# Optimization experiments

Hardware: AMD Instinct MI355X
Metric: run time of the kernel (lower is better)

The kernel has to match this reference:

```python
import jax, jax.numpy as jnp
import numpy as np

DEPTH, DIM, DIN, DM, NST, RNK, CSTEM, NCLS = 4, 64, 128, 256, 16, 8, 32, 16
EPS = 1e-5


def silu(x):
    return x * jax.nn.sigmoid(x)


def layernorm(x, g, b):
    m = x.mean(-1, keepdims=True)
    v = x.var(-1, keepdims=True)
    return (x - m) / jnp.sqrt(v + EPS) * g + b


def bn3d(x, g, b, m, v):  # eval-mode BatchNorm3d, x [B,C,T,H,W]
    s = g / jnp.sqrt(v + EPS)
    return x * s[None, :, None, None, None] + (b - m * s)[None, :, None, None, None]


def dwconv3d_same(x, w, b):  # x [B,C,T,H,W], w [C,1,3,3,3]
    y = jax.lax.conv_general_dilated(x, w, (1, 1, 1), 'SAME',
                                     feature_group_count=x.shape[1],
                                     dimension_numbers=('NCDHW', 'OIDHW', 'NCDHW'))
    return y + b[None, :, None, None, None]


def mamba(u, in_w, conv_w, conv_b, xproj_w, dtproj_w, dtproj_b, Alog, Dp, out_w):
    # u: [b, L, DIN]; mamba_ssm Mamba(d_model=DIN, d_state=16, expand=2, d_conv=4)
    b, L, _ = u.shape
    xz = u @ in_w.T                                  # [b,L,2*DM]
    x, z = jnp.split(xz, 2, axis=-1)                 # [b,L,DM] each
    # causal depthwise conv1d, kernel 4, left-pad 3
    xc = jnp.moveaxis(x, 1, 2)                       # [b,DM,L]
    xc = jnp.pad(xc, ((0, 0), (0, 0), (3, 0)))
    xc = jax.lax.conv_general_dilated(xc, conv_w, (1,), 'VALID',
                                      feature_group_count=conv_w.shape[0],
                                      dimension_numbers=('NCH', 'OIH', 'NCH'))
    xc = xc + conv_b[None, :, None]
    x = silu(jnp.moveaxis(xc, 2, 1))                 # [b,L,DM]
    dbc = x @ xproj_w.T                              # [b,L,RNK+2*NST]
    dt, Bc, Cc = jnp.split(dbc, [RNK, RNK + NST], axis=-1)
    dt = jax.nn.softplus(dt @ dtproj_w.T + dtproj_b)  # [b,L,DM]
    A = -jnp.exp(Alog)                               # [DM,NST]

    def step(h, inp):
        dt_l, u_l, B_l, C_l = inp                    # [b,DM],[b,DM],[b,NST],[b,NST]
        dA = jnp.exp(dt_l[..., None] * A)            # [b,DM,NST]
        h = dA * h + (dt_l * u_l)[..., None] * B_l[:, None, :]
        y = jnp.einsum('bdn,bn->bd', h, C_l)
        return h, y

    xs = (jnp.moveaxis(dt, 1, 0), jnp.moveaxis(x, 1, 0),
          jnp.moveaxis(Bc, 1, 0), jnp.moveaxis(Cc, 1, 0))
    h0 = jnp.zeros((b, DM, NST), x.dtype)
    _, ys = jax.lax.scan(step, h0, xs)               # ys [L,b,DM]
    y = jnp.moveaxis(ys, 0, 1) + x * Dp              # D skip
    y = y * silu(z)
    return y @ out_w.T                               # [b,L,DIN]


def setup_inputs() -> dict:
    key = jax.random.key(0)
    ks = iter(jax.random.split(key, 64))

    def rn(shape, s=0.02):
        return jax.random.normal(next(ks), shape, jnp.float32) * s

    D = DEPTH
    inp = {
        'x': jax.random.normal(next(ks), (32, 1, 32, 13, 13), jnp.float32),
        # R(2+1)D stem
        'sconv_w': rn((CSTEM, 1, 1, 3, 3), 0.1),
        'bn1_g': jnp.ones((CSTEM,)), 'bn1_b': jnp.zeros((CSTEM,)),
        'bn1_m': rn((CSTEM,), 0.1),
        'bn1_v': jax.random.uniform(next(ks), (CSTEM,), jnp.float32, 0.5, 1.5),
        'tconv_w': rn((CSTEM, 1, 3, 1, 1), 0.2),
        'bn2_g': jnp.ones((CSTEM,)), 'bn2_b': jnp.zeros((CSTEM,)),
        'bn2_m': rn((CSTEM,), 0.1),
        'bn2_v': jax.random.uniform(next(ks), (CSTEM,), jnp.float32, 0.5, 1.5),
        'last_w': rn((2 * CSTEM, CSTEM, 1, 1, 1), 0.1),
        # per-block params, stacked over depth
        'ln1_g': jnp.ones((D, DIM)), 'ln1_b': jnp.zeros((D, DIM)),
        'in_proj_w': rn((D, 2 * DIN, DIM)),
        'conv3d_w': rn((D, DIN, 1, 3, 3, 3), 0.1), 'conv3d_b': rn((D, DIN), 0.1),
        'm_in_w': rn((D, 2 * DM, DIN)),
        'm_conv_w': rn((D, DM, 1, 4), 0.2), 'm_conv_b': rn((D, DM), 0.1),
        'm_xproj_w': rn((D, RNK + 2 * NST, DM)),
        'm_dtproj_w': rn((D, DM, RNK), 0.1), 'm_dtproj_b': rn((D, DM), 0.1),
        'm_Alog': jnp.log(jax.random.uniform(next(ks), (D, DM, NST), jnp.float32, 1.0, 16.0)),
        'm_D': jnp.ones((D, DM)),
        'm_out_w': rn((D, DIN, DM)),
        'out_proj_w': rn((D, DIM, DIN)),
        'ln2_g': jnp.ones((D, DIM)), 'ln2_b': jnp.zeros((D, DIM)),
        'fc1_w': rn((D, 4 * DIM, DIM)), 'fc1_b': rn((D, 4 * DIM), 0.1),
        'fc2_w': rn((D, DIM, 4 * DIM)), 'fc2_b': rn((D, DIM), 0.1),
        'head_w': rn((NCLS, DIM)), 'head_b': jnp.zeros((NCLS,)),
    }
    return inp


def reference(x, sconv_w, bn1_g, bn1_b, bn1_m, bn1_v, tconv_w, bn2_g, bn2_b, bn2_m,
              bn2_v, last_w, ln1_g, ln1_b, in_proj_w, conv3d_w, conv3d_b, m_in_w,
              m_conv_w, m_conv_b, m_xproj_w, m_dtproj_w, m_dtproj_b, m_Alog, m_D,
              m_out_w, out_proj_w, ln2_g, ln2_b, fc1_w, fc1_b, fc2_w, fc2_b,
              head_w, head_b):
    dn = ('NCDHW', 'OIDHW', 'NCDHW')
    # R(2+1)D stem: spatial conv -> BN -> ReLU -> temporal dwconv -> BN -> ReLU -> 1x1x1
    h = jax.lax.conv_general_dilated(x, sconv_w, (1, 1, 1), 'VALID', dimension_numbers=dn)
    h = jax.nn.relu(bn3d(h, bn1_g, bn1_b, bn1_m, bn1_v))
    h = jax.lax.conv_general_dilated(h, tconv_w, (1, 1, 1), 'VALID',
                                     feature_group_count=CSTEM, dimension_numbers=dn)
    h = jax.nn.relu(bn3d(h, bn2_g, bn2_b, bn2_m, bn2_v))
    h = jax.lax.conv_general_dilated(h, last_w, (1, 1, 1), 'VALID', dimension_numbers=dn)
    xb = jnp.transpose(h, (0, 2, 3, 4, 1))  # [B, T', H', W', DIM]

    for i in range(DEPTH):
        # --- SSM branch ---
        hx = layernorm(xb, ln1_g[i], ln1_b[i])
        xz = hx @ in_proj_w[i].T                       # [B,T,H,W,2*DIN]
        xs_, z = jnp.split(xz, 2, axis=-1)
        z = silu(z)
        xc = jnp.moveaxis(xs_, 4, 1)                   # [B,DIN,T,H,W]
        xc = silu(dwconv3d_same(xc, conv3d_w[i], conv3d_b[i]))
        b, c, t, hh, ww = xc.shape
        seq = jnp.moveaxis(xc.reshape(b, c, t * hh * ww), 1, 2)  # [B,L,DIN]
        seq2 = jnp.concatenate([seq, seq[:, ::-1]], axis=0)      # [2B,L,DIN]
        y2 = mamba(seq2, m_in_w[i], m_conv_w[i], m_conv_b[i], m_xproj_w[i],
                   m_dtproj_w[i], m_dtproj_b[i], m_Alog[i], m_D[i], m_out_w[i])
        y = y2[:b] + y2[b:, ::-1]
        y = y.reshape(b, t, hh, ww, c) * z
        xb = xb + y @ out_proj_w[i].T
        # --- MLP branch ---
        h2 = layernorm(xb, ln2_g[i], ln2_b[i])
        h2 = jax.nn.gelu(h2 @ fc1_w[i].T + fc1_b[i], approximate=False)
        xb = xb + h2 @ fc2_w[i].T + fc2_b[i]

    feature = xb.mean(axis=(1, 2, 3))                  # [B, DIM]
    logits = feature @ head_w.T + head_b               # [B, NCLS]
    return (logits, feature)
```

## Files before the change

kernel.cpp:

```cpp
#include <hip/hip_runtime.h>
#include <hip/hip_bf16.h>
#include <hip/hip_fp16.h>

#define LL    3630
#define EPSV  1e-5f
#define NCH   33
#define CLEN  110

typedef short bf16x8 __attribute__((ext_vector_type(8)));
typedef float f32x4  __attribute__((ext_vector_type(4)));
typedef float f32x2  __attribute__((ext_vector_type(2)));
typedef float f32x16 __attribute__((ext_vector_type(16)));

__device__ __forceinline__ float bf2f(__hip_bfloat16 x){ return __bfloat162float(x); }
__device__ __forceinline__ __hip_bfloat16 f2bf(float x){ return __float2bfloat16(x); }
__device__ __forceinline__ float siluf(float x){ return x / (1.f + __expf(-x)); }
__device__ __forceinline__ float s2f(short s){ __hip_bfloat16 t = __builtin_bit_cast(__hip_bfloat16, s); return __bfloat162float(t); }
__device__ __forceinline__ short f2s(float x){ __hip_bfloat16 t = __float2bfloat16(x); return __builtin_bit_cast(short, t); }

__global__ __launch_bounds__(256) void convert_weights(
    const float* __restrict__ s0, const float* __restrict__ s1,
    const float* __restrict__ s2, const float* __restrict__ s3,
    const float* __restrict__ s4, const float* __restrict__ s5,
    const float* __restrict__ s6,
    __hip_bfloat16* __restrict__ dst)
{
  int gid = blockIdx.x*256 + threadIdx.x;
  float v;
  if      (gid <  65536) v = s0[gid];
  else if (gid < 327680) v = s1[gid-65536];
  else if (gid < 458752) v = s2[gid-327680];
  else if (gid < 491520) v = s3[gid-458752];
  else if (gid < 557056) v = s4[gid-491520];
  else if (gid < 622592) v = s5[gid-557056];
  else if (gid < 671744){
    int rel = gid - 622592;
    int layer = rel / 12288;
    int rr  = (rel % 12288) / 256;
    int ccol= rel & 255;
    v = (rr < 40) ? s6[layer*10240 + rr*256 + ccol] : 0.f;
  }
  else return;
  dst[gid] = f2bf(v);
}

__global__ __launch_bounds__(256) void stem1_kernel(
    const float* __restrict__ x, const float* __restrict__ w,
    const float* __restrict__ g, const float* __restrict__ bb,
    const float* __restrict__ mm, const float* __restrict__ vv,
    float* __restrict__ out, int nb, int b0)
{
  int idx = blockIdx.x*256 + threadIdx.x;
  if (idx >= nb*123904) return;
  int j = idx % 11;
  int i = (idx/11) % 11;
  int t = (idx/121) % 32;
  int c = (idx/(121*32)) % 32;
  int b = idx/(121*32*32);
  const float* xp = x + ((b0+b)*32 + t)*169;
  const float* wp = w + c*9;
  float acc = 0.f;
  #pragma unroll
  for (int di=0; di<3; ++di)
    #pragma unroll
    for (int dj=0; dj<3; ++dj)
      acc += xp[(i+di)*13 + (j+dj)] * wp[di*3+dj];
  float s = g[c]*rsqrtf(vv[c]+EPSV);
  acc = acc*s + (bb[c]-mm[c]*s);
  out[idx] = fmaxf(acc, 0.f);
}

__global__ __launch_bounds__(256) void stem2_kernel(
    const float* __restrict__ h1, const float* __restrict__ w,
    const float* __restrict__ g, const float* __restrict__ bb,
    const float* __restrict__ mm, const float* __restrict__ vv,
    float* __restrict__ out, int nb)
{
  int idx = blockIdx.x*256 + threadIdx.x;
  if (idx >= nb*116160) return;
  int ij = idx % 121;
  int t  = (idx/121) % 30;
  int c  = (idx/(121*30)) % 32;
  int b  = idx/(121*30*32);
  const float* hp = h1 + ((b*32+c)*32)*121 + ij;
  const float* wp = w + c*3;
  float acc = 0.f;
  #pragma unroll
  for (int k=0;k<3;++k) acc += hp[(t+k)*121] * wp[k];
  float s = g[c]*rsqrtf(vv[c]+EPSV);
  acc = acc*s + (bb[c]-mm[c]*s);
  out[idx] = fmaxf(acc, 0.f);
}

__global__ __launch_bounds__(256) void stem3_kernel(
    const float* __restrict__ h2, const float* __restrict__ w,
    __hip_bfloat16* __restrict__ xb, int tokens)
{
  int gid = blockIdx.x*256 + threadIdx.x;
  int cc = gid & 63;
  int tok = gid >> 6;
  if (tok >= tokens) return;
  int ij = tok % 121;
  int t  = (tok/121) % 30;
  int b  = tok/LL;
  const float* hp = h2 + ((long)b*32)*30*121 + t*121 + ij;
  const float* wp = w + cc*32;
  float acc = 0.f;
  #pragma unroll
  for (int ci=0; ci<32; ++ci) acc += hp[ci*3630] * wp[ci];
  xb[(long)tok*64+cc] = f2bf(acc);
}

__global__ __launch_bounds__(256) void ln_kernel(
    const __hip_bfloat16* __restrict__ xb, const float* __restrict__ g,
    const float* __restrict__ b2, __hip_bfloat16* __restrict__ out, int tokens)
{
  int wid = threadIdx.x >> 6, lane = threadIdx.x & 63;
  long tok = (long)blockIdx.x*4 + wid;
  if (tok >= tokens) return;
  float v = bf2f(xb[tok*64 + lane]);
  float s = v, q = v*v;
  #pragma unroll
  for (int m=1; m<64; m<<=1){ s += __shfl_xor(s,m); q += __shfl_xor(q,m); }
  float mean = s*(1.f/64.f);
  float var  = q*(1.f/64.f) - mean*mean;
  float o = (v-mean)*rsqrtf(var+EPSV)*g[lane] + b2[lane];
  out[tok*64+lane] = f2bf(o);
}

template<int EPI>
__global__ __launch_bounds__(256) void gemm_bf16(
    const __hip_bfloat16* __restrict__ A, const __hip_bfloat16* __restrict__ W,
    int K, int N, int NH, int tokens,
    __hip_bfloat16* __restrict__ out1, __hip_bfloat16* __restrict__ out2,
    const float* __restrict__ bias, const __hip_bfloat16* __restrict__ gate,
    __hip_bfloat16* __restrict__ resid,
    const float* __restrict__ lng, const float* __restrict__ lnb)
{
  int w   = threadIdx.x >> 6;
  int lane= threadIdx.x & 63;
  int r16 = lane & 15;
  int kg  = lane >> 4;
  long m0 = (long)blockIdx.x*128 + w*32;
  int  n0 = blockIdx.y*64;
  long ra0 = m0 + r16;      if (ra0 > tokens-1) ra0 = tokens-1;
  long ra1 = m0 + 16 + r16; if (ra1 > tokens-1) ra1 = tokens-1;
  f32x4 acc[2][4] = { { {0,0,0,0},{0,0,0,0},{0,0,0,0},{0,0,0,0} },
                      { {0,0,0,0},{0,0,0,0},{0,0,0,0},{0,0,0,0} } };
  for (int k0 = 0; k0 < K; k0 += 32){
    bf16x8 a0 = *reinterpret_cast<const bf16x8*>(A + ra0*K + k0 + kg*8);
    bf16x8 a1 = *reinterpret_cast<const bf16x8*>(A + ra1*K + k0 + kg*8);
    #pragma unroll
    for (int f=0; f<4; ++f){
      bf16x8 b = *reinterpret_cast<const bf16x8*>(W + (long)(n0 + f*16 + r16)*K + k0 + kg*8);
      acc[0][f] = __builtin_amdgcn_mfma_f32_16x16x32_bf16(a0, b, acc[0][f], 0, 0, 0);
      acc[1][f] = __builtin_amdgcn_mfma_f32_16x16x32_bf16(a1, b, acc[1][f], 0, 0, 0);
    }
  }
  if (EPI == 5){
    float gv[4], bv[4], biasv[4];
    #pragma unroll
    for (int f=0; f<4; ++f){
      gv[f] = lng[f*16+r16]; bv[f] = lnb[f*16+r16];
      biasv[f] = bias ? bias[f*16+r16] : 0.f;
    }
    #pragma unroll
    for (int g2=0; g2<2; ++g2){
      #pragma unroll
      for (int r=0; r<4; ++r){
        long row = m0 + g2*16 + kg*4 + r;
        bool ok = row < tokens;
        long rowc = ok ? row : (tokens-1);
        float v[4]; float s = 0.f, q = 0.f;
        #pragma unroll
        for (int f=0; f<4; ++f){
          float t = acc[g2][f][r] + biasv[f] + bf2f(resid[rowc*64 + f*16+r16]);
          v[f] = t; s += t; q += t*t;
        }
        #pragma unroll
        for (int m=1; m<16; m<<=1){ s += __shfl_xor(s,m); q += __shfl_xor(q,m); }
        float mean = s*(1.f/64.f);
        float var  = q*(1.f/64.f) - mean*mean;
        float rstd = rsqrtf(var+EPSV);
        if (ok){
          #pragma unroll
          for (int f=0; f<4; ++f){
            resid[row*64 + f*16+r16] = f2bf(v[f]);
            out1 [row*64 + f*16+r16] = f2bf((v[f]-mean)*rstd*gv[f] + bv[f]);
          }
        }
      }
    }
    return;
  }
  #pragma unroll
  for (int g2=0; g2<2; ++g2){
    #pragma unroll
    for (int f=0; f<4; ++f){
      int col = n0 + f*16 + r16;
      #pragma unroll
      for (int r=0; r<4; ++r){
        long row = m0 + g2*16 + kg*4 + r;
        if (row >= tokens) continue;
        float v = acc[g2][f][r];
        if (EPI == 0){
          if (col < NH) out1[row*NH + col] = f2bf(v);
          else          out2[row*NH + col - NH] = f2bf(siluf(v));
        } else if (EPI == 2){
          v += bias[col];
          v = 0.5f*v*(1.f + erff(v*0.70710678118f));
          out1[row*N + col] = f2bf(v);
        } else if (EPI == 3){
          if (bias) v += bias[col];
          resid[row*N + col] = f2bf(v + bf2f(resid[row*N + col]));
        } else {
          out1[row*N + col] = f2bf(v * bf2f(gate[row*N + col]));
        }
      }
    }
  }
}

__global__ __launch_bounds__(256) void dwconv3d_kernel(
    const __hip_bfloat16* __restrict__ xs, const float* __restrict__ w,
    const float* __restrict__ bias, __hip_bfloat16* __restrict__ seq, int tokens)
{
  long gid = (long)blockIdx.x*256 + threadIdx.x;
  int c = gid & 127;
  long tok = gid >> 7;
  if (tok >= tokens) return;
  int j  = tok % 11;
  int i2 = (tok/11) % 11;
  int t  = (tok/121) % 30;
  long b = tok/LL;
  const float* wc = w + c*27;
  float acc = bias[c];
  #pragma unroll
  for (int dt=0; dt<3; ++dt){
    int tt = t+dt-1; if (tt<0 || tt>=30) continue;
    #pragma unroll
    for (int di=0; di<3; ++di){
      int ii = i2+di-1; if (ii<0 || ii>=11) continue;
      #pragma unroll
      for (int dj=0; dj<3; ++dj){
        int jj = j+dj-1; if (jj<0 || jj>=11) continue;
        long t2 = (b*30+tt)*121 + ii*11 + jj;
        acc += wc[dt*9+di*3+dj] * bf2f(xs[t2*128 + c]);
      }
    }
  }
  seq[tok*128 + c] = f2bf(siluf(acc));
}

__global__ __launch_bounds__(256) void mamba_pre_kernel(
    const __hip_bfloat16* __restrict__ xm,
    const float* __restrict__ cw, const float* __restrict__ cbv,
    const __hip_bfloat16* __restrict__ xpw_bf,
    __hip_bfloat16* __restrict__ ub,
    float* __restrict__ pre,
    int nb)
{
  __shared__ __hip_bfloat16 xcs[64][264];
  int s  = blockIdx.x / 57;
  int ch = blockIdx.x % 57;
  int p0 = ch*64;
  int b  = s % nb;
  bool fwd = s < nb;
  int d = threadIdx.x;
  const long basex = (long)b*LL*256 + d;
  const long sLL = (long)s*LL;
  float w0=cw[d*4], w1=cw[d*4+1], w2=cw[d*4+2], w3=cw[d*4+3], cb=cbv[d];
  float p1=0.f, p2=0.f, p3=0.f;
  if (p0-1 >= 0) p1 = bf2f(xm[basex + (long)(fwd ? p0-1 : LL-p0  )*256]);
  if (p0-2 >= 0) p2 = bf2f(xm[basex + (long)(fwd ? p0-2 : LL+1-p0)*256]);
  if (p0-3 >= 0) p3 = bf2f(xm[basex + (long)(fwd ? p0-3 : LL+2-p0)*256]);
  for (int t=0; t<64; ++t){
    int p = p0 + t;
    float xl = 0.f;
    if (p < LL) xl = bf2f(xm[basex + (long)(fwd ? p : LL-1-p)*256]);
    float xc = w3*xl + w2*p1 + w1*p2 + w0*p3 + cb;
    p3=p2; p2=p1; p1=xl;
    __hip_bfloat16 uv = f2bf(siluf(xc));
    xcs[t][d] = uv;
    if (p < LL) ub[(sLL + p)*256 + d] = uv;
  }
  __syncthreads();
  int w = threadIdx.x >> 6, lane = threadIdx.x & 63;
  int r16 = lane & 15, kg = lane >> 4;
  int t0 = w*16;
  f32x4 acc[3] = { {0,0,0,0},{0,0,0,0},{0,0,0,0} };
  for (int k0=0; k0<256; k0+=32){
    bf16x8 a = *reinterpret_cast<const bf16x8*>(&xcs[t0+r16][k0+kg*8]);
    #pragma unroll
    for (int f=0; f<3; ++f){
      bf16x8 bb = *reinterpret_cast<const bf16x8*>(xpw_bf + (f*16+r16)*256 + k0 + kg*8);
      acc[f] = __builtin_amdgcn_mfma_f32_16x16x32_bf16(a, bb, acc[f], 0, 0, 0);
    }
  }
  #pragma unroll
  for (int f=0; f<3; ++f){
    int col = f*16 + r16;
    #pragma unroll
    for (int r=0; r<4; ++r){
      int tl = t0 + kg*4 + r;
      int p = p0 + tl;
      if (p >= LL) continue;
      if (col < 40) pre[(sLL + p)*40 + col] = acc[f][r];
    }
  }
}

__global__ __launch_bounds__(256) void scan_p1(
    const __hip_bfloat16* __restrict__ ub,
    const float* __restrict__ pre,
    const float* __restrict__ dtw, const float* __restrict__ dtbv,
    const float* __restrict__ Alog,
    float* __restrict__ hfin, float* __restrict__ sdt)
{
  int d = threadIdx.x;
  int sc = blockIdx.x;
  int ch = sc % NCH, s = sc / NCH;
  f32x2 a2[8], h[8];
  #pragma unroll
  for (int k=0;k<8;++k){
    a2[k] = (f32x2){ -__expf(Alog[d*16+2*k])*1.44269504f,
                     -__expf(Alog[d*16+2*k+1])*1.44269504f };
    h[k] = (f32x2){0.f, 0.f};
  }
  float dw[8];
  #pragma unroll
  for (int r=0;r<8;++r) dw[r] = dtw[d*8+r];
  float dtb_d = dtbv[d];
  float sacc = 0.f;
  long tok0 = (long)s*LL + ch*CLEN;
  long ui = tok0*256 + d;
  long pi = tok0*40;
  for (int l=0; l<CLEN; ++l){
    float u = bf2f(ub[ui]);
    float4 r0 = *reinterpret_cast<const float4*>(pre+pi);
    float4 r1 = *reinterpret_cast<const float4*>(pre+pi+4);
    float xacc = dtb_d;
    xacc = fmaf(r0.x,dw[0],fmaf(r0.y,dw[1],fmaf(r0.z,dw[2],fmaf(r0.w,dw[3],xacc))));
    xacc = fmaf(r1.x,dw[4],fmaf(r1.y,dw[5],fmaf(r1.z,dw[6],fmaf(r1.w,dw[7],xacc))));
    float dt = (xacc > 20.f) ? xacc : __logf(1.f + __expf(xacc));
    sacc += dt;
    f32x16 B = *reinterpret_cast<const f32x16*>(pre+pi+8);
    f32x2 dt2  = (f32x2){dt, dt};
    float dtu = dt*u;
    f32x2 dtu2 = (f32x2){dtu, dtu};
    #pragma unroll
    for (int k=0;k<8;++k){
      f32x2 t = dt2*a2[k];
      f32x2 e = (f32x2){ exp2f(t.x), exp2f(t.y) };
      f32x2 bk = (f32x2){ B[2*k], B[2*k+1] };
      h[k] = __builtin_elementwise_fma(e, h[k], dtu2*bk);
    }
    ui += 256; pi += 40;
  }
  long hbase = ((long)sc*256 + d)*16;
  #pragma unroll
  for (int k=0;k<8;++k){ hfin[hbase+2*k] = h[k].x; hfin[hbase+2*k+1] = h[k].y; }
  sdt[(long)sc*256 + d] = sacc;
}

__global__ __launch_bounds__(256) void scan_comb(
    const float* __restrict__ Alog,
    float* __restrict__ hfin, const float* __restrict__ sdt)
{
  int s = blockIdx.x >> 4, dg = blockIdx.x & 15;
  int d = dg*16 + (threadIdx.x >> 4), n = threadIdx.x & 15;
  float a2 = -__expf(Alog[d*16+n]) * 1.44269504f;
  float h = 0.f;
  for (int ch=0; ch<NCH; ++ch){
    long sc = (long)s*NCH + ch;
    long idx = (sc*256 + d)*16 + n;
    float hf = hfin[idx];
    float sd = sdt[sc*256 + d];
    hfin[idx] = h;
    h = exp2f(a2*sd)*h + hf;
  }
}

__global__ __launch_bounds__(256) void scan_p2(
    __hip_bfloat16* __restrict__ ub,
    const float* __restrict__ pre,
    const float* __restrict__ dtw, const float* __restrict__ dtbv,
    const float* __restrict__ Alog, const float* __restrict__ Dv,
    const float* __restrict__ hinit)
{
  int d = threadIdx.x;
  int sc = blockIdx.x;
  int ch = sc % NCH, s = sc / NCH;
  f32x2 a2[8], h[8];
  long hbase = ((long)sc*256 + d)*16;
  #pragma unroll
  for (int k=0;k<8;++k){
    a2[k] = (f32x2){ -__expf(Alog[d*16+2*k])*1.44269504f,
                     -__expf(Alog[d*16+2*k+1])*1.44269504f };
    h[k] = (f32x2){ hinit[hbase+2*k], hinit[hbase+2*k+1] };
  }
  float dw[8];
  #pragma unroll
  for (int r=0;r<8;++r) dw[r] = dtw[d*8+r];
  float dtb_d = dtbv[d];
  float dpv = Dv[d];
  int l0 = ch*CLEN;
  long tok0 = (long)s*LL + l0;
  long ui = tok0*256 + d;
  long pi = tok0*40;
  for (int l=0; l<CLEN; ++l){
    float u = bf2f(ub[ui]);
    float4 r0 = *reinterpret_cast<const float4*>(pre+pi);
    float4 r1 = *reinterpret_cast<const float4*>(pre+pi+4);
    float xacc = dtb_d;
    xacc = fmaf(r0.x,dw[0],fmaf(r0.y,dw[1],fmaf(r0.z,dw[2],fmaf(r0.w,dw[3],xacc))));
    xacc = fmaf(r1.x,dw[4],fmaf(r1.y,dw[5],fmaf(r1.z,dw[6],fmaf(r1.w,dw[7],xacc))));
    float dt = (xacc > 20.f) ? xacc : __logf(1.f + __expf(xacc));
    f32x16 B = *reinterpret_cast<const f32x16*>(pre+pi+8);
    f32x16 C = *reinterpret_cast<const f32x16*>(pre+pi+24);
    f32x2 dt2  = (f32x2){dt, dt};
    float dtu = dt*u;
    f32x2 dtu2 = (f32x2){dtu, dtu};
    f32x2 y2 = (f32x2){0.f, 0.f};
    #pragma unroll
    for (int k=0;k<8;++k){
      f32x2 t = dt2*a2[k];
      f32x2 e = (f32x2){ exp2f(t.x), exp2f(t.y) };
      f32x2 bk = (f32x2){ B[2*k], B[2*k+1] };
      f32x2 ck = (f32x2){ C[2*k], C[2*k+1] };
      h[k] = __builtin_elementwise_fma(e, h[k], dtu2*bk);
      y2 = __builtin_elementwise_fma(h[k], ck, y2);
    }
    float y = y2.x + y2.y;
    ub[ui] = f2bf(y + u*dpv);
    ui += 256; pi += 40;
  }
}

__global__ __launch_bounds__(256) void combine_kernel(
    const __hip_bfloat16* __restrict__ yb, const __hip_bfloat16* __restrict__ zm,
    __hip_bfloat16* __restrict__ ycomb, int tokens, int nb)
{
  long gid = (long)blockIdx.x*256 + threadIdx.x;
  long tok = gid >> 5;
  if (tok >= tokens) return;
  int c8 = (gid & 31) * 8;
  long l = tok % LL, b = tok / LL;
  bf16x8 vf = *reinterpret_cast<const bf16x8*>(yb + ( b*LL + l)*256 + c8);
  bf16x8 vb = *reinterpret_cast<const bf16x8*>(yb + ((nb+b)*LL + (LL-1-l))*256 + c8);
  bf16x8 zz = *reinterpret_cast<const bf16x8*>(zm + tok*256 + c8);
  bf16x8 out;
  #pragma unroll
  for (int k=0;k<8;++k){
    float r = (s2f(vf[k]) + s2f(vb[k])) * s2f(zz[k]);
    out[k] = f2s(r);
  }
  *reinterpret_cast<bf16x8*>(ycomb + tok*256 + c8) = out;
}

__global__ __launch_bounds__(256) void head1_kernel(
    const __hip_bfloat16* __restrict__ xb, float* __restrict__ hp)
{
  __shared__ float partial[4][64];
  int b = blockIdx.x / 30, ch = blockIdx.x % 30;
  int d = threadIdx.x & 63, part = threadIdx.x >> 6;
  float acc = 0.f;
  int lend = (ch+1)*121;
  for (int l = ch*121 + part; l < lend; l += 4)
    acc += bf2f(xb[((long)b*LL + l)*64 + d]);
  partial[part][d] = acc;
  __syncthreads();
  if (part == 0)
    hp[(b*30 + ch)*64 + d] = partial[0][d]+partial[1][d]+partial[2][d]+partial[3][d];
}

__global__ __launch_bounds__(64) void head2_kernel(
    const float* __restrict__ hp, const float* __restrict__ hw,
    const float* __restrict__ hb, float* __restrict__ out, int b0)
{
  __shared__ float feat[64];
  int b = blockIdx.x;
  int d = threadIdx.x;
  float acc = 0.f;
  #pragma unroll
  for (int ch=0; ch<30; ++ch) acc += hp[(b*30+ch)*64 + d];
  float f = acc * (1.f/3630.f);
  feat[d] = f;
  out[512 + (b0+b)*64 + d] = f;
  __syncthreads();
  if (d < 16){
    float a2 = hb[d];
    #pragma unroll
    for (int k=0; k<64; ++k) a2 += feat[k]*hw[d*64+k];
    out[(b0+b)*16 + d] = a2;
  }
}

extern "C" void kernel_launch(void* const* d_in, const int* in_sizes, int n_in,
                              void* d_out, int out_size, void* d_ws, size_t ws_size,
                              hipStream_t stream)
{
  const float* x        = (const float*)d_in[0];
  const float* sconv_w  = (const float*)d_in[1];
  const float* bn1_g    = (const float*)d_in[2];
  const float* bn1_b    = (const float*)d_in[3];
  const float* bn1_m    = (const float*)d_in[4];
  const float* bn1_v    = (const float*)d_in[5];
  const float* tconv_w  = (const float*)d_in[6];
  const float* bn2_g    = (const float*)d_in[7];
  const float* bn2_b    = (const float*)d_in[8];
  const float* bn2_m    = (const float*)d_in[9];
  const float* bn2_v    = (const float*)d_in[10];
  const float* last_w   = (const float*)d_in[11];
  const float* ln1_g    = (const float*)d_in[12];
  const float* ln1_b    = (const float*)d_in[13];
  const float* in_proj_w= (const float*)d_in[14];
  const float* conv3d_w = (const float*)d_in[15];
  const float* conv3d_b = (const float*)d_in[16];
  const float* m_in_w   = (const float*)d_in[17];
  const float* m_conv_w = (const float*)d_in[18];
  const float* m_conv_b = (const float*)d_in[19];
  const float* m_xproj_w= (const float*)d_in[20];
  const float* m_dtproj_w=(const float*)d_in[21];
  const float* m_dtproj_b=(const float*)d_in[22];
  const float* m_Alog   = (const float*)d_in[23];
  const float* m_D      = (const float*)d_in[24];
  const float* m_out_w  = (const float*)d_in[25];
  const float* out_proj_w=(const float*)d_in[26];
  const float* ln2_g    = (const float*)d_in[27];
  const float* ln2_b    = (const float*)d_in[28];
  const float* fc1_w    = (const float*)d_in[29];
  const float* fc1_b    = (const float*)d_in[30];
  const float* fc2_w    = (const float*)d_in[31];
  const float* fc2_b    = (const float*)d_in[32];
  const float* head_w   = (const float*)d_in[33];
  const float* head_b   = (const float*)d_in[34];

  const size_t WB = 1345536;
  int nb = 1;
  for (int cand = 32; cand >= 1; cand >>= 1){
    size_t TPc = (((size_t)cand*LL + 63)/64)*64;
    size_t S2c = (size_t)2*cand*LL;
    size_t need = WB + TPc*2048 + S2c*672;
    if (need <= ws_size){ nb = cand; break; }
  }
  const size_t TP  = (((size_t)nb*LL + 63)/64)*64;
  const int S2  = 2*nb;
  const size_t S2T = (size_t)S2*LL;
  const int tokens = nb*LL;

  char* ws = (char*)d_ws;
  __hip_bfloat16* wbf   = (__hip_bfloat16*)(ws);
  size_t o = WB;
  __hip_bfloat16* xb    = (__hip_bfloat16*)(ws + o); o += TP*128;
  __hip_bfloat16* hx    = (__hip_bfloat16*)(ws + o); o += TP*128;
  float*          hp    = (float*)hx;
  __hip_bfloat16* xs    = (__hip_bfloat16*)(ws + o); o += TP*256;
  __hip_bfloat16* seq   = (__hip_bfloat16*)(ws + o); o += TP*256;
  __hip_bfloat16* ycomb = xs;
  float*          hfin  = (float*)xs;
  __hip_bfloat16* zblk  = (__hip_bfloat16*)(ws + o); o += TP*256;
  __hip_bfloat16* xm    = (__hip_bfloat16*)(ws + o);
  __hip_bfloat16* yo    = xm;                        o += TP*512;
  __hip_bfloat16* zm    = (__hip_bfloat16*)(ws + o);
  __hip_bfloat16* h2m   = zm;                        o += TP*512;
  float*          pre   = (float*)(ws + o);          o += S2T*160;
  __hip_bfloat16* ybuf  = (__hip_bfloat16*)(ws + o);
  float*          h1s   = (float*)(ws + o);
  float*          h2s   = (float*)(ws + o + (size_t)nb*495616);
  float*          sdtb  = hfin + (size_t)S2*NCH*4096;

  convert_weights<<<2624, 256, 0, stream>>>(in_proj_w, m_in_w, m_out_w, out_proj_w,
                                            fc1_w, fc2_w, m_xproj_w, wbf);

  const int gM2 = (int)((TP + 127)/128);

  for (int b0 = 0; b0 < 32; b0 += nb){
    stem1_kernel<<<nb*484, 256, 0, stream>>>(x, sconv_w, bn1_g, bn1_b, bn1_m, bn1_v, h1s, nb, b0);
    stem2_kernel<<<(nb*116160+255)/256, 256, 0, stream>>>(h1s, tconv_w, bn2_g, bn2_b, bn2_m, bn2_v, h2s, nb);
    stem3_kernel<<<(tokens*64+255)/256, 256, 0, stream>>>(h2s, last_w, xb, tokens);
    ln_kernel<<<(tokens+3)/4, 256, 0, stream>>>(xb, ln1_g, ln1_b, hx, tokens);

    for (int i = 0; i < 4; ++i){
      gemm_bf16<0><<<dim3(gM2,4), 256, 0, stream>>>(hx, wbf + i*16384, 64, 256, 128, tokens,
                                                    xs, zblk, nullptr, nullptr, nullptr, nullptr, nullptr);
      dwconv3d_kernel<<<(tokens*128+255)/256, 256, 0, stream>>>(xs, conv3d_w + i*3456, conv3d_b + i*128, seq, tokens);
      gemm_bf16<0><<<dim3(gM2,8), 256, 0, stream>>>(seq, wbf + 65536 + i*65536, 128, 512, 256, tokens,
                                                    xm, zm, nullptr, nullptr, nullptr, nullptr, nullptr);
      mamba_pre_kernel<<<S2*57, 256, 0, stream>>>(xm, m_conv_w + i*1024, m_conv_b + i*256,
                                                  wbf + 622592 + i*12288, ybuf, pre, nb);
      scan_p1<<<S2*NCH, 256, 0, stream>>>(ybuf, pre, m_dtproj_w + i*2048, m_dtproj_b + i*256,
                                          m_Alog + i*4096, hfin, sdtb);
      scan_comb<<<S2*16, 256, 0, stream>>>(m_Alog + i*4096, hfin, sdtb);
      scan_p2<<<S2*NCH, 256, 0, stream>>>(ybuf, pre, m_dtproj_w + i*2048, m_dtproj_b + i*256,
                                          m_Alog + i*4096, m_D + i*256, hfin);
      combine_kernel<<<(tokens*32+255)/256, 256, 0, stream>>>(ybuf, zm, ycomb, tokens, nb);
      gemm_bf16<4><<<dim3(gM2,2), 256, 0, stream>>>(ycomb, wbf + 327680 + i*32768, 256, 128, 0, tokens,
                                                    yo, nullptr, nullptr, zblk, nullptr, nullptr, nullptr);
      gemm_bf16<5><<<dim3(gM2,1), 256, 0, stream>>>(yo, wbf + 458752 + i*8192, 128, 64, 0, tokens,
                                                    hx, nullptr, nullptr, nullptr, xb,
                                                    ln2_g + i*64, ln2_b + i*64);
      gemm_bf16<2><<<dim3(gM2,4), 256, 0, stream>>>(hx, wbf + 491520 + i*16384, 64, 256, 0, tokens,
                                                    h2m, nullptr, fc1_b + i*256, nullptr, nullptr, nullptr, nullptr);
      int inext = (i < 3) ? i+1 : 3;
      gemm_bf16<5><<<dim3(gM2,1), 256, 0, stream>>>(h2m, wbf + 557056 + i*16384, 256, 64, 0, tokens,
                                                    hx, nullptr, fc2_b + i*64, nullptr, xb,
                                                    ln1_g + inext*64, ln1_b + inext*64);
    }
    head1_kernel<<<nb*30, 256, 0, stream>>>(xb, hp);
    head2_kernel<<<nb, 64, 0, stream>>>(hp, head_w, head_b, (float*)d_out, b0);
  }
}
```

Before: 6.706 ms.

## Fuse mamba pre-projection with chunked scan phase one using shared-memory inputs

Merges the conv1d+x_proj kernel with the first pass of the chunked selective scan. The scan now reads u and the dt/B projections from shared memory instead of global memory. Chunk length changes from 110 to 64 to match the pre-kernel tiling, giving 57 chunks per sequence. This removes a launch and a global re-read of ub/pre. In exchange it lengthens the sequential scan_comb pass and enlarges the hfin buffer, which is moved to alias a different workspace region.

After: 6.192 ms. 7.7% less time.

```diff
diff --git a/kernel.cpp b/kernel.cpp
--- a/kernel.cpp
+++ b/kernel.cpp
@@ -4,8 +4,8 @@
 
 #define LL    3630
 #define EPSV  1e-5f
-#define NCH   33
-#define CLEN  110
+#define NCH   57
+#define CLEN  64
 
 typedef short bf16x8 __attribute__((ext_vector_type(8)));
 typedef float f32x4  __attribute__((ext_vector_type(4)));
@@ -252,115 +252,118 @@
   seq[tok*128 + c] = f2bf(siluf(acc));
 }
 
-__global__ __launch_bounds__(256) void mamba_pre_kernel(
+__global__ __launch_bounds__(256) void mamba_pre_scan(
     const __hip_bfloat16* __restrict__ xm,
     const float* __restrict__ cw, const float* __restrict__ cbv,
     const __hip_bfloat16* __restrict__ xpw_bf,
+    const float* __restrict__ dtw, const float* __restrict__ dtbv,
+    const float* __restrict__ Alog,
     __hip_bfloat16* __restrict__ ub,
     float* __restrict__ pre,
+    float* __restrict__ hfin, float* __restrict__ sdt,
     int nb)
 {
   __shared__ __hip_bfloat16 xcs[64][264];
-  int s  = blockIdx.x / 57;
-  int ch = blockIdx.x % 57;
-  int p0 = ch*64;
+  __shared__ float pres[64][44];
+  int s  = blockIdx.x / NCH;
+  int ch = blockIdx.x % NCH;
+  int p0 = ch*CLEN;
   int b  = s % nb;
   bool fwd = s < nb;
   int d = threadIdx.x;
   const long basex = (long)b*LL*256 + d;
   const long sLL = (long)s*LL;
-  float w0=cw[d*4], w1=cw[d*4+1], w2=cw[d*4+2], w3=cw[d*4+3], cb=cbv[d];
-  float p1=0.f, p2=0.f, p3=0.f;
-  if (p0-1 >= 0) p1 = bf2f(xm[basex + (long)(fwd ? p0-1 : LL-p0  )*256]);
-  if (p0-2 >= 0) p2 = bf2f(xm[basex + (long)(fwd ? p0-2 : LL+1-p0)*256]);
-  if (p0-3 >= 0) p3 = bf2f(xm[basex + (long)(fwd ? p0-3 : LL+2-p0)*256]);
-  for (int t=0; t<64; ++t){
-    int p = p0 + t;
-    float xl = 0.f;
-    if (p < LL) xl = bf2f(xm[basex + (long)(fwd ? p : LL-1-p)*256]);
-    float xc = w3*xl + w2*p1 + w1*p2 + w0*p3 + cb;
-    p3=p2; p2=p1; p1=xl;
-    __hip_bfloat16 uv = f2bf(siluf(xc));
-    xcs[t][d] = uv;
-    if (p < LL) ub[(sLL + p)*256 + d] = uv;
+  {
+    float w0=cw[d*4], w1=cw[d*4+1], w2=cw[d*4+2], w3=cw[d*4+3], cb=cbv[d];
+    float p1=0.f, p2=0.f, p3=0.f;
+    if (p0-1 >= 0) p1 = bf2f(xm[basex + (long)(fwd ? p0-1 : LL-p0  )*256]);
+    if (p0-2 >= 0) p2 = bf2f(xm[basex + (long)(fwd ? p0-2 : LL+1-p0)*256]);
+    if (p0-3 >= 0) p3 = bf2f(xm[basex + (long)(fwd ? p0-3 : LL+2-p0)*256]);
+    for (int t=0; t<64; ++t){
+      int p = p0 + t;
+      float xl = 0.f;
+      if (p < LL) xl = bf2f(xm[basex + (long)(fwd ? p : LL-1-p)*256]);
+      float xc = w3*xl + w2*p1 + w1*p2 + w0*p3 + cb;
+      p3=p2; p2=p1; p1=xl;
+      __hip_bfloat16 uv = f2bf(siluf(xc));
+      xcs[t][d] = uv;
+      if (p < LL) ub[(sLL + p)*256 + d] = uv;
+    }
   }
   __syncthreads();
-  int w = threadIdx.x >> 6, lane = threadIdx.x & 63;
-  int r16 = lane & 15, kg = lane >> 4;
-  int t0 = w*16;
-  f32x4 acc[3] = { {0,0,0,0},{0,0,0,0},{0,0,0,0} };
-  for (int k0=0; k0<256; k0+=32){
-    bf16x8 a = *reinterpret_cast<const bf16x8*>(&xcs[t0+r16][k0+kg*8]);
+  {
+    int w = threadIdx.x >> 6, lane = threadIdx.x & 63;
+    int r16 = lane & 15, kg = lane >> 4;
+    int t0 = w*16;
+    f32x4 acc[3] = { {0,0,0,0},{0,0,0,0},{0,0,0,0} };
+    for (int k0=0; k0<256; k0+=32){
+      bf16x8 a = *reinterpret_cast<const bf16x8*>(&xcs[t0+r16][k0+kg*8]);
+      #pragma unroll
+      for (int f=0; f<3; ++f){
+        bf16x8 bb = *reinterpret_cast<const bf16x8*>(xpw_bf + (f*16+r16)*256 + k0 + kg*8);
+        acc[f] = __builtin_amdgcn_mfma_f32_16x16x32_bf16(a, bb, acc[f], 0, 0, 0);
+      }
+    }
     #pragma unroll
     for (int f=0; f<3; ++f){
-      bf16x8 bb = *reinterpret_cast<const bf16x8*>(xpw_bf + (f*16+r16)*256 + k0 + kg*8);
-      acc[f] = __builtin_amdgcn_mfma_f32_16x16x32_bf16(a, bb, acc[f], 0, 0, 0);
-    }
-  }
-  #pragma unroll
-  for (int f=0; f<3; ++f){
-    int col = f*16 + r16;
-    #pragma unroll
-    for (int r=0; r<4; ++r){
-      int tl = t0 + kg*4 + r;
-      int p = p0 + tl;
-      if (p >= LL) continue;
-      if (col < 40) pre[(sLL + p)*40 + col] = acc[f][r];
-    }
-  }
-}
-
-__global__ __launch_bounds__(256) void scan_p1(
-    const __hip_bfloat16* __restrict__ ub,
-    const float* __restrict__ pre,
-    const float* __restrict__ dtw, const float* __restrict__ dtbv,
-    const float* __restrict__ Alog,
-    float* __restrict__ hfin, float* __restrict__ sdt)
-{
-  int d = threadIdx.x;
-  int sc = blockIdx.x;
-  int ch = sc % NCH, s = sc / NCH;
-  f32x2 a2[8], h[8];
-  #pragma unroll
-  for (int k=0;k<8;++k){
-    a2[k] = (f32x2){ -__expf(Alog[d*16+2*k])*1.44269504f,
-                     -__expf(Alog[d*16+2*k+1])*1.44269504f };
-    h[k] = (f32x2){0.f, 0.f};
-  }
-  float dw[8];
-  #pragma unroll
-  for (int r=0;r<8;++r) dw[r] = dtw[d*8+r];
-  float dtb_d = dtbv[d];
-  float sacc = 0.f;
-  long tok0 = (long)s*LL + ch*CLEN;
-  long ui = tok0*256 + d;
-  long pi = tok0*40;
-  for (int l=0; l<CLEN; ++l){
-    float u = bf2f(ub[ui]);
-    float4 r0 = *reinterpret_cast<const float4*>(pre+pi);
-    float4 r1 = *reinterpret_cast<const float4*>(pre+pi+4);
-    float xacc = dtb_d;
-    xacc = fmaf(r0.x,dw[0],fmaf(r0.y,dw[1],fmaf(r0.z,dw[2],fmaf(r0.w,dw[3],xacc))));
-    xacc = fmaf(r1.x,dw[4],fmaf(r1.y,dw[5],fmaf(r1.z,dw[6],fmaf(r1.w,dw[7],xacc))));
-    float dt = (xacc > 20.f) ? xacc : __logf(1.f + __expf(xacc));
-    sacc += dt;
-    f32x16 B = *reinterpret_cast<const f32x16*>(pre+pi+8);
-    f32x2 dt2  = (f32x2){dt, dt};
-    float dtu = dt*u;
-    f32x2 dtu2 = (f32x2){dtu, dtu};
+      int col = f*16 + r16;
+      #pragma unroll
+      for (int r=0; r<4; ++r){
+        int tl = t0 + kg*4 + r;
+        int p = p0 + tl;
+        if (col < 40){
+          pres[tl][col] = acc[f][r];
+          if (p < LL) pre[(sLL + p)*40 + col] = acc[f][r];
+        }
+      }
+    }
+  }
+  __syncthreads();
+  {
+    int lim = LL - p0; if (lim > CLEN) lim = CLEN;
+    f32x2 a2[8], h[8];
     #pragma unroll
     for (int k=0;k<8;++k){
-      f32x2 t = dt2*a2[k];
-      f32x2 e = (f32x2){ exp2f(t.x), exp2f(t.y) };
-      f32x2 bk = (f32x2){ B[2*k], B[2*k+1] };
-      h[k] = __builtin_elementwise_fma(e, h[k], dtu2*bk);
-    }
-    ui += 256; pi += 40;
-  }
-  long hbase = ((long)sc*256 + d)*16;
-  #pragma unroll
-  for (int k=0;k<8;++k){ hfin[hbase+2*k] = h[k].x; hfin[hbase+2*k+1] = h[k].y; }
-  sdt[(long)sc*256 + d] = sacc;
+      a2[k] = (f32x2){ -__expf(Alog[d*16+2*k])*1.44269504f,
+                       -__expf(Alog[d*16+2*k+1])*1.44269504f };
+      h[k] = (f32x2){0.f, 0.f};
+    }
+    float dw[8];
+    #pragma unroll
+    for (int r=0;r<8;++r) dw[r] = dtw[d*8+r];
+    float dtb_d = dtbv[d];
+    float sacc = 0.f;
+    for (int t=0; t<lim; ++t){
+      float u = bf2f(xcs[t][d]);
+      float4 r0 = *reinterpret_cast<const float4*>(&pres[t][0]);
+      float4 r1 = *reinterpret_cast<const float4*>(&pres[t][4]);
+      float xacc = dtb_d;
+      xacc = fmaf(r0.x,dw[0],fmaf(r0.y,dw[1],fmaf(r0.z,dw[2],fmaf(r0.w,dw[3],xacc))));
+      xacc = fmaf(r1.x,dw[4],fmaf(r1.y,dw[5],fmaf(r1.z,dw[6],fmaf(r1.w,dw[7],xacc))));
+      float dt = (xacc > 20.f) ? xacc : __logf(1.f + __expf(xacc));
+      sacc += dt;
+      float4 B0 = *reinterpret_cast<const float4*>(&pres[t][8]);
+      float4 B1 = *reinterpret_cast<const float4*>(&pres[t][12]);
+      float4 B2 = *reinterpret_cast<const float4*>(&pres[t][16]);
+      float4 B3 = *reinterpret_cast<const float4*>(&pres[t][20]);
+      float Bv[16] = {B0.x,B0.y,B0.z,B0.w,B1.x,B1.y,B1.z,B1.w,
+                      B2.x,B2.y,B2.z,B2.w,B3.x,B3.y,B3.z,B3.w};
+      f32x2 dt2  = (f32x2){dt, dt};
+      float dtu = dt*u;
+      f32x2 dtu2 = (f32x2){dtu, dtu};
+      #pragma unroll
+      for (int k=0;k<8;++k){
+        f32x2 tt = dt2*a2[k];
+        f32x2 e = (f32x2){ exp2f(tt.x), exp2f(tt.y) };
+        f32x2 bk = (f32x2){ Bv[2*k], Bv[2*k+1] };
+        h[k] = __builtin_elementwise_fma(e, h[k], dtu2*bk);
+      }
+    }
+    long hbase = ((long)blockIdx.x*256 + d)*16;
+    #pragma unroll
+    for (int k=0;k<8;++k){ hfin[hbase+2*k] = h[k].x; hfin[hbase+2*k+1] = h[k].y; }
+    sdt[(long)blockIdx.x*256 + d] = sacc;
+  }
 }
 
 __global__ __launch_bounds__(256) void scan_comb(
@@ -391,6 +394,8 @@
   int d = threadIdx.x;
   int sc = blockIdx.x;
   int ch = sc % NCH, s = sc / NCH;
+  int l0 = ch*CLEN;
+  int lim = LL - l0; if (lim > CLEN) lim = CLEN;
   f32x2 a2[8], h[8];
   long hbase = ((long)sc*256 + d)*16;
   #pragma unroll
@@ -404,11 +409,10 @@
   for (int r=0;r<8;++r) dw[r] = dtw[d*8+r];
   float dtb_d = dtbv[d];
   float dpv = Dv[d];
-  int l0 = ch*CLEN;
   long tok0 = (long)s*LL + l0;
   long ui = tok0*256 + d;
   long pi = tok0*40;
-  for (int l=0; l<CLEN; ++l){
+  for (int l=0; l<lim; ++l){
     float u = bf2f(ub[ui]);
     float4 r0 = *reinterpret_cast<const float4*>(pre+pi);
     float4 r1 = *reinterpret_cast<const float4*>(pre+pi+4);
@@ -555,10 +559,10 @@
   __hip_bfloat16* xb    = (__hip_bfloat16*)(ws + o); o += TP*128;
   __hip_bfloat16* hx    = (__hip_bfloat16*)(ws + o); o += TP*128;
   float*          hp    = (float*)hx;
+  float*          hfin  = (float*)hx;
   __hip_bfloat16* xs    = (__hip_bfloat16*)(ws + o); o += TP*256;
   __hip_bfloat16* seq   = (__hip_bfloat16*)(ws + o); o += TP*256;
   __hip_bfloat16* ycomb = xs;
-  float*          hfin  = (float*)xs;
   __hip_bfloat16* zblk  = (__hip_bfloat16*)(ws + o); o += TP*256;
   __hip_bfloat16* xm    = (__hip_bfloat16*)(ws + o);
   __hip_bfloat16* yo    = xm;                        o += TP*512;
@@ -587,10 +591,11 @@
       dwconv3d_kernel<<<(tokens*128+255)/256, 256, 0, stream>>>(xs, conv3d_w + i*3456, conv3d_b + i*128, seq, tokens);
       gemm_bf16<0><<<dim3(gM2,8), 256, 0, stream>>>(seq, wbf + 65536 + i*65536, 128, 512, 256, tokens,
                                                     xm, zm, nullptr, nullptr, nullptr, nullptr, nullptr);
-      mamba_pre_kernel<<<S2*57, 256, 0, stream>>>(xm, m_conv_w + i*1024, m_conv_b + i*256,
-                                                  wbf + 622592 + i*12288, ybuf, pre, nb);
-      scan_p1<<<S2*NCH, 256, 0, stream>>>(ybuf, pre, m_dtproj_w + i*2048, m_dtproj_b + i*256,
-                                          m_Alog + i*4096, hfin, sdtb);
+      mamba_pre_scan<<<S2*NCH, 256, 0, stream>>>(xm, m_conv_w + i*1024, m_conv_b + i*256,
+                                                 wbf + 622592 + i*12288,
+                                                 m_dtproj_w + i*2048, m_dtproj_b + i*256,
+                                                 m_Alog + i*4096,
+                                                 ybuf, pre, hfin, sdtb, nb);
       scan_comb<<<S2*16, 256, 0, stream>>>(m_Alog + i*4096, hfin, sdtb);
       scan_p2<<<S2*NCH, 256, 0, stream>>>(ybuf, pre, m_dtproj_w + i*2048, m_dtproj_b + i*256,
                                           m_Alog + i*4096, m_D + i*256, hfin);
```
